# Optimization experiments

Measured on AMD Instinct MI355X. Metric: run time of the kernel, lower is better.

The kernel has to match this reference:

```python
import jax, jax.numpy as jnp
import numpy as np

E = 1024      # emb_dim
H = 16        # num_heads
DH = E // H   # per-head atten_dim
B = 2
T = 2048


def _layernorm(x, scale, shift, eps=1e-5):
    mean = x.mean(axis=-1, keepdims=True)
    var = ((x - mean) ** 2).mean(axis=-1, keepdims=True)  # unbiased=False
    return scale * (x - mean) / jnp.sqrt(var + eps) + shift


def _gelu(x):
    # Faithful to source: tanh(sqrt(2/pi)*x + 0.044715*x^3)  (no sqrt on cubic term)
    c = jnp.sqrt(jnp.asarray(2.0 / jnp.pi, x.dtype))
    return 0.5 * x * (1.0 + jnp.tanh(c * x + 0.044715 * x ** 3))


def setup_inputs() -> dict:
    key = jax.random.key(0)
    ks = jax.random.split(key, 12)
    s = 0.02
    return {
        "x":     jax.random.normal(ks[0], (B, T, E), jnp.float32),
        "Wq":    jax.random.normal(ks[1], (H, E, DH), jnp.float32) * s,
        "Wk":    jax.random.normal(ks[2], (H, E, DH), jnp.float32) * s,
        "Wv":    jax.random.normal(ks[3], (H, E, DH), jnp.float32) * s,
        "fc_w":  jax.random.normal(ks[4], (E, E), jnp.float32) * s,
        "fc_b":  jnp.zeros((E,), jnp.float32),
        "ln1_s": jnp.ones((E,), jnp.float32),
        "ln1_b": jnp.zeros((E,), jnp.float32),
        "ln2_s": jnp.ones((E,), jnp.float32),
        "ln2_b": jnp.zeros((E,), jnp.float32),
        "ff_w1": jax.random.normal(ks[5], (E, 4 * E), jnp.float32) * s,
        "ff_b1": jnp.zeros((4 * E,), jnp.float32),
        "ff_w2": jax.random.normal(ks[6], (4 * E, E), jnp.float32) * s,
        "ff_b2": jnp.zeros((E,), jnp.float32),
    }


def _attention(x, Wq, Wk, Wv, fc_w, fc_b):
    b, t, _ = x.shape
    q = jnp.einsum("bte,hed->bhtd", x, Wq)
    k = jnp.einsum("bte,hed->bhtd", x, Wk)
    v = jnp.einsum("bte,hed->bhtd", x, Wv)
    scores = jnp.einsum("bhtd,bhsd->bhts", q, k)
    causal = jnp.triu(jnp.ones((t, t), bool), 1)
    scores = jnp.where(causal, -jnp.inf, scores)
    w = jax.nn.softmax(scores / jnp.sqrt(jnp.asarray(DH, x.dtype)), axis=-1)
    ctx = jnp.einsum("bhts,bhsd->bhtd", w, v)
    # faithful quirk from source: per-head transpose(1,2) then reshape(b, T, d_out)
    ctx = jnp.swapaxes(ctx, 2, 3).reshape(b, H, t, DH)
    concat = ctx.transpose(0, 2, 1, 3).reshape(b, t, E)
    return concat @ fc_w + fc_b


def reference(x, Wq, Wk, Wv, fc_w, fc_b, ln1_s, ln1_b, ln2_s, ln2_b,
              ff_w1, ff_b1, ff_w2, ff_b2):
    h = _attention(_layernorm(x, ln1_s, ln1_b), Wq, Wk, Wv, fc_w, fc_b) + x
    y = _layernorm(h, ln2_s, ln2_b)
    y = _gelu(y @ ff_w1 + ff_b1) @ ff_w2 + ff_b2
    return y + h
```

## Files before the change

### kernel.cpp

```cpp
#include <hip/hip_runtime.h>


#define En 1024
#define Hn 16
#define DHn 64
#define Bn 2
#define Tn 2048
#define Mrows 4096

typedef __attribute__((ext_vector_type(8))) short bf16x8;
typedef __attribute__((ext_vector_type(4))) float f32x4;

__device__ __forceinline__ short f2bf(float f) {
    unsigned u = __float_as_uint(f);
    u += 0x7FFFu + ((u >> 16) & 1u);
    return (short)(u >> 16);
}
__device__ __forceinline__ ushort f2bfu(float f) {
    unsigned u = __float_as_uint(f);
    u += 0x7FFFu + ((u >> 16) & 1u);
    return (ushort)(u >> 16);
}

__device__ __forceinline__ float gelu_f(float x) {
    float u = 0.79788456080286535588f * x + 0.044715f * x * x * x;
    float t = __expf(2.0f * u);
    return x * t / (t + 1.0f);
}

__device__ __forceinline__ void load_lds16(const void* g, void* l) {
    __builtin_amdgcn_global_load_lds(
        (const __attribute__((address_space(1))) unsigned int*)(uintptr_t)g,
        (__attribute__((address_space(3))) unsigned int*)(uintptr_t)l,
        16, 0, 0);
}

__global__ __launch_bounds__(256) void ln_kernel(
    const float* __restrict__ in, const float* __restrict__ sc,
    const float* __restrict__ sh, ushort* __restrict__ out)
{
    int row = blockIdx.x;
    int tid = threadIdx.x;
    float4 v = ((const float4*)(in + (size_t)row * En))[tid];
    float s  = v.x + v.y + v.z + v.w;
    float s2 = v.x*v.x + v.y*v.y + v.z*v.z + v.w*v.w;
    #pragma unroll
    for (int off = 32; off > 0; off >>= 1) {
        s  += __shfl_down(s,  off);
        s2 += __shfl_down(s2, off);
    }
    __shared__ float red[2][4];
    int wave = tid >> 6, lane = tid & 63;
    if (lane == 0) { red[0][wave] = s; red[1][wave] = s2; }
    __syncthreads();
    s  = red[0][0] + red[0][1] + red[0][2] + red[0][3];
    s2 = red[1][0] + red[1][1] + red[1][2] + red[1][3];
    float mean = s * (1.0f / En);
    float var  = s2 * (1.0f / En) - mean * mean;
    float r = rsqrtf(var + 1e-5f);
    float4 scv = ((const float4*)sc)[tid];
    float4 shv = ((const float4*)sh)[tid];
    ushort4 o;
    o.x = f2bfu(scv.x * (v.x - mean) * r + shv.x);
    o.y = f2bfu(scv.y * (v.y - mean) * r + shv.y);
    o.z = f2bfu(scv.z * (v.z - mean) * r + shv.z);
    o.w = f2bfu(scv.w * (v.w - mean) * r + shv.w);
    ((ushort4*)(out + (size_t)row * En))[tid] = o;
}

__global__ __launch_bounds__(256) void ln2_fuse(
    const float* __restrict__ P0, const float* __restrict__ P1,
    const float* __restrict__ bias, const float* __restrict__ x,
    const float* __restrict__ sc, const float* __restrict__ sh,
    float* __restrict__ hb, ushort* __restrict__ ynb)
{
    int row = blockIdx.x, tid = threadIdx.x;
    size_t idx = (size_t)row * 256 + tid;
    float4 a  = ((const float4*)P0)[idx];
    float4 b  = ((const float4*)P1)[idx];
    float4 bi = ((const float4*)bias)[tid];
    float4 xr = ((const float4*)x)[idx];
    float4 v;
    v.x = a.x + b.x + bi.x + xr.x;
    v.y = a.y + b.y + bi.y + xr.y;
    v.z = a.z + b.z + bi.z + xr.z;
    v.w = a.w + b.w + bi.w + xr.w;
    ((float4*)hb)[idx] = v;
    float s  = v.x + v.y + v.z + v.w;
    float s2 = v.x*v.x + v.y*v.y + v.z*v.z + v.w*v.w;
    #pragma unroll
    for (int off = 32; off > 0; off >>= 1) {
        s  += __shfl_down(s,  off);
        s2 += __shfl_down(s2, off);
    }
    __shared__ float red[2][4];
    int wave = tid >> 6, lane = tid & 63;
    if (lane == 0) { red[0][wave] = s; red[1][wave] = s2; }
    __syncthreads();
    s  = red[0][0] + red[0][1] + red[0][2] + red[0][3];
    s2 = red[1][0] + red[1][1] + red[1][2] + red[1][3];
    float mean = s * (1.0f / En);
    float var  = s2 * (1.0f / En) - mean * mean;
    float r = rsqrtf(var + 1e-5f);
    float4 scv = ((const float4*)sc)[tid];
    float4 shv = ((const float4*)sh)[tid];
    ushort4 o;
    o.x = f2bfu(scv.x * (v.x - mean) * r + shv.x);
    o.y = f2bfu(scv.y * (v.y - mean) * r + shv.y);
    o.z = f2bfu(scv.z * (v.z - mean) * r + shv.z);
    o.w = f2bfu(scv.w * (v.w - mean) * r + shv.w);
    ((ushort4*)ynb)[idx] = o;
}

__global__ __launch_bounds__(256) void ff2_reduce(
    const float* __restrict__ P0, const float* __restrict__ P1,
    const float* __restrict__ bias, const float* __restrict__ hb,
    float* __restrict__ out)
{
    int tid = threadIdx.x;
    size_t i = (size_t)blockIdx.x * 256 + tid;
    float4 a  = ((const float4*)P0)[i];
    float4 b  = ((const float4*)P1)[i];
    float4 bi = ((const float4*)bias)[tid];
    float4 h  = ((const float4*)hb)[i];
    float4 o;
    o.x = a.x + b.x + bi.x + h.x;
    o.y = a.y + b.y + bi.y + h.y;
    o.z = a.z + b.z + bi.z + h.z;
    o.w = a.w + b.w + bi.w + h.w;
    ((float4*)out)[i] = o;
}

__global__ __launch_bounds__(256) void transpose_w(
    const float* __restrict__ in, ushort* __restrict__ out, int K, int N)
{
    __shared__ float t[64][65];
    int k0 = blockIdx.x * 64, n0 = blockIdx.y * 64;
    int tid = threadIdx.x, r = tid >> 4, c4 = (tid & 15) * 4;
    #pragma unroll
    for (int i = 0; i < 4; ++i) {
        float4 v = *(const float4*)(in + (size_t)(k0 + r + i * 16) * N + n0 + c4);
        t[r + i * 16][c4 + 0] = v.x; t[r + i * 16][c4 + 1] = v.y;
        t[r + i * 16][c4 + 2] = v.z; t[r + i * 16][c4 + 3] = v.w;
    }
    __syncthreads();
    #pragma unroll
    for (int i = 0; i < 4; ++i) {
        int n = r + i * 16;
        ushort4 u;
        u.x = f2bfu(t[c4 + 0][n]); u.y = f2bfu(t[c4 + 1][n]);
        u.z = f2bfu(t[c4 + 2][n]); u.w = f2bfu(t[c4 + 3][n]);
        *(ushort4*)(out + (size_t)(n0 + n) * K + k0 + c4) = u;
    }
}

__global__ __launch_bounds__(256) void transpose_qkv(
    const float* __restrict__ Wq, const float* __restrict__ Wk,
    const float* __restrict__ Wv, ushort* __restrict__ out)
{
    __shared__ float t[64][65];
    int z = blockIdx.z, sel = z >> 4, h = z & 15;
    const float* in = (sel == 0 ? Wq : sel == 1 ? Wk : Wv) + (size_t)h * En * DHn;
    ushort* o = out + ((size_t)(sel * 1024 + h * 64)) * En;
    int k0 = blockIdx.x * 64;
    int tid = threadIdx.x, r = tid >> 4, c4 = (tid & 15) * 4;
    #pragma unroll
    for (int i = 0; i < 4; ++i) {
        float4 v = *(const float4*)(in + (size_t)(k0 + r + i * 16) * DHn + c4);
        t[r + i * 16][c4 + 0] = v.x; t[r + i * 16][c4 + 1] = v.y;
        t[r + i * 16][c4 + 2] = v.z; t[r + i * 16][c4 + 3] = v.w;
    }
    __syncthreads();
    #pragma unroll
    for (int i = 0; i < 4; ++i) {
        int n = r + i * 16;
        ushort4 u;
        u.x = f2bfu(t[c4 + 0][n]); u.y = f2bfu(t[c4 + 1][n]);
        u.z = f2bfu(t[c4 + 2][n]); u.w = f2bfu(t[c4 + 3][n]);
        *(ushort4*)(o + (size_t)n * En + k0 + c4) = u;
    }
}

template<int MODE, int TN>
__global__ __launch_bounds__(256) void gemm_bf16(
    const ushort* __restrict__ A, int lda,
    const ushort* __restrict__ Bt, int ldb, int Kloop,
    const float* __restrict__ bias,
    float* __restrict__ Cf, ushort* __restrict__ Cb, int ldc,
    ushort* __restrict__ qo, ushort* __restrict__ ko, ushort* __restrict__ vo)
{
    constexpr int WCN = TN / 2;
    constexpr int NI  = WCN / 16;
    constexpr int BIW = TN * 8 / 256;
    __shared__ ushort As[128 * 64];
    __shared__ ushort Bs[TN * 64];
    int tid = threadIdx.x, wv = tid >> 6, lid = tid & 63;
    int m0 = blockIdx.x * 128, n0 = blockIdx.y * TN;
    int koff = blockIdx.z * Kloop;
    int wr = wv >> 1, wc = wv & 1;
    int hm = lid & 15, hk = lid >> 4;

    f32x4 acc[4][NI];
    #pragma unroll
    for (int i = 0; i < 4; ++i)
        #pragma unroll
        for (int j = 0; j < NI; ++j) acc[i][j] = (f32x4){0.f, 0.f, 0.f, 0.f};

    const ushort* Abase = A + (size_t)m0 * lda + koff;
    const ushort* Bbase = Bt + (size_t)n0 * ldb + koff;

    for (int k0 = 0; k0 < Kloop; k0 += 64) {
        __syncthreads();
        #pragma unroll
        for (int i = 0; i < 4; ++i) {
            int c = wv * 256 + i * 64 + lid;
            int r = c >> 3, s = c & 7;
            int j = s ^ (r & 7);
            load_lds16(Abase + (size_t)r * lda + k0 + j * 8,
                       &As[(wv * 256 + i * 64) * 8]);
        }
        #pragma unroll
        for (int i = 0; i < BIW; ++i) {
            int c = wv * (BIW * 64) + i * 64 + lid;
            int r = c >> 3, s = c & 7;
            int j = s ^ (r & 7);
            load_lds16(Bbase + (size_t)r * ldb + k0 + j * 8,
                       &Bs[(wv * (BIW * 64) + i * 64) * 8]);
        }
        __syncthreads();
        #pragma unroll
        for (int kk = 0; kk < 2; ++kk) {
            bf16x8 af[4], bfr[NI];
            #pragma unroll
            for (int mi = 0; mi < 4; ++mi) {
                int r = wr * 64 + mi * 16 + hm;
                int slot = ((kk << 2) | hk) ^ (r & 7);
                af[mi] = *(const bf16x8*)&As[(r * 8 + slot) * 8];
            }
            #pragma unroll
            for (int ni = 0; ni < NI; ++ni) {
                int r = wc * WCN + ni * 16 + hm;
                int slot = ((kk << 2) | hk) ^ (r & 7);
                bfr[ni] = *(const bf16x8*)&Bs[(r * 8 + slot) * 8];
            }
            #pragma unroll
            for (int mi = 0; mi < 4; ++mi)
                #pragma unroll
                for (int ni = 0; ni < NI; ++ni)
                    acc[mi][ni] = __builtin_amdgcn_mfma_f32_16x16x32_bf16(
                        af[mi], bfr[ni], acc[mi][ni], 0, 0, 0);
        }
    }

    int colbase = n0 + wc * WCN + hm;
    int rowbase = m0 + wr * 64 + hk * 4;
    if (MODE == 1) {
        #pragma unroll
        for (int ni = 0; ni < NI; ++ni) {
            int col = colbase + ni * 16;
            float bb = bias[col];
            #pragma unroll
            for (int mi = 0; mi < 4; ++mi) {
                int row = rowbase + mi * 16;
                #pragma unroll
                for (int r = 0; r < 4; ++r)
                    Cb[(size_t)(row + r) * ldc + col] =
                        f2bfu(gelu_f(acc[mi][ni][r] + bb));
            }
        }
    } else if (MODE == 2) {
        #pragma unroll
        for (int ni = 0; ni < NI; ++ni) {
            int col = colbase + ni * 16;
            int sel = col >> 10, cc = col & 1023;
            int h = cc >> 6, d = cc & 63;
            if (sel < 2) {
                ushort* outp = (sel == 0 ? qo : ko)
                             + (size_t)h * (Mrows * DHn) + d;
                #pragma unroll
                for (int mi = 0; mi < 4; ++mi) {
                    int row = rowbase + mi * 16;
                    #pragma unroll
                    for (int r = 0; r < 4; ++r)
                        outp[(size_t)(row + r) * DHn] = f2bfu(acc[mi][ni][r]);
                }
            } else {
                #pragma unroll
                for (int mi = 0; mi < 4; ++mi) {
                    int row = rowbase + mi * 16;
                    int bb2 = row >> 11, t = row & 2047;
                    ushort4 u;
                    u.x = f2bfu(acc[mi][ni][0]); u.y = f2bfu(acc[mi][ni][1]);
                    u.z = f2bfu(acc[mi][ni][2]); u.w = f2bfu(acc[mi][ni][3]);
                    *(ushort4*)(vo + ((size_t)((h * 2 + bb2) * 64 + d)) * Tn + t) = u;
                }
            }
        }
    } else {
        float* Cp = Cf + (size_t)blockIdx.z * Mrows * ldc;
        #pragma unroll
        for (int ni = 0; ni < NI; ++ni) {
            int col = colbase + ni * 16;
            #pragma unroll
            for (int mi = 0; mi < 4; ++mi) {
                int row = rowbase + mi * 16;
                #pragma unroll
                for (int r = 0; r < 4; ++r)
                    Cp[(size_t)(row + r) * ldc + col] = acc[mi][ni][r];
            }
        }
    }
}

__global__ __launch_bounds__(256) void attn_mfma(
    const ushort* __restrict__ q, const ushort* __restrict__ ksrc,
    const ushort* __restrict__ vtsrc, ushort* __restrict__ cat)
{
    int g = blockIdx.x;
    int h = g >> 1, b = g & 1;
    const ushort* qg  = q     + (size_t)g * Tn * DHn;
    const ushort* kg  = ksrc  + (size_t)g * Tn * DHn;
    const ushort* vtg = vtsrc + (size_t)g * DHn * Tn;
    int tid = threadIdx.x, wave = tid >> 6, lane = tid & 63;
    int m = lane & 15, gq = lane >> 4;

    __shared__ short Ks[4096];
    __shared__ short Vt[4096];
    __shared__ short Ps[4][1024];

    int R  = tid >> 2;
    int c2 = tid & 3;

    #pragma unroll 1
    for (int phase = 0; phase < 2; ++phase) {
        int qt = phase ? (31 - (int)blockIdx.y) : (int)blockIdx.y;
        int q0 = qt * 64;

        bf16x8 qf[2];
        {
            const ushort* qp = qg + (size_t)(q0 + wave * 16 + m) * DHn + gq * 8;
            qf[0] = *(const bf16x8*)(qp);
            qf[1] = *(const bf16x8*)(qp + 32);
        }
        f32x4 o[4];
        #pragma unroll
        for (int i = 0; i < 4; ++i) o[i] = (f32x4){0.f, 0.f, 0.f, 0.f};
        float lsum[4] = {0.f, 0.f, 0.f, 0.f};

        for (int kt = 0; kt <= qt; ++kt) {
            int k0 = kt * 64;
            __syncthreads();
            {
                const ushort* ksp = kg  + (size_t)(k0 + R) * DHn + c2 * 16;
                const ushort* vsp = vtg + (size_t)R * Tn + k0 + c2 * 16;
                bf16x8 f0 = *(const bf16x8*)(ksp);
                bf16x8 f1 = *(const bf16x8*)(ksp + 8);
                bf16x8 v0 = *(const bf16x8*)(vsp);
                bf16x8 v1 = *(const bf16x8*)(vsp + 8);
                *(bf16x8*)&Ks[R * 64 + (((c2 * 2    ) ^ (R & 7)) << 3)] = f0;
                *(bf16x8*)&Ks[R * 64 + (((c2 * 2 + 1) ^ (R & 7)) << 3)] = f1;
                *(bf16x8*)&Vt[R * 64 + (((c2 * 2    ) ^ (R & 7)) << 3)] = v0;
                *(bf16x8*)&Vt[R * 64 + (((c2 * 2 + 1) ^ (R & 7)) << 3)] = v1;
            }
            __syncthreads();

            bool diag = (kt == qt);
            float ps[4][4];
            #pragma unroll
            for (int ct = 0; ct < 4; ++ct) {
                if (diag && ct > wave) {
                    ps[ct][0] = ps[ct][1] = ps[ct][2] = ps[ct][3] = 0.f;
                    continue;
                }
                f32x4 acc = (f32x4){0.f, 0.f, 0.f, 0.f};
                int row = ct * 16 + m;
                #pragma unroll
                for (int db = 0; db < 2; ++db) {
                    bf16x8 kf = *(const bf16x8*)&Ks[row * 64 + (((db * 4 + gq) ^ (row & 7)) << 3)];
                    acc = __builtin_amdgcn_mfma_f32_16x16x32_bf16(qf[db], kf, acc, 0, 0, 0);
                }
                #pragma unroll
                for (int r = 0; r < 4; ++r) {
                    float p;
                    if (diag && (ct * 16 + m) > (wave * 16 + gq * 4 + r)) {
                        p = 0.f;
                    } else {
                        p = __expf(acc[r] * 0.125f);
                    }
                    ps[ct][r] = p;
                    lsum[r] += p;
                }
            }

            #pragma unroll
            for (int ct = 0; ct < 4; ++ct)
                #pragma unroll
                for (int r = 0; r < 4; ++r) {
                    int row = gq * 4 + r;
                    Ps[wave][row * 64 + ((((ct * 2 + (m >> 3)) ^ (row & 7)) << 3) | (m & 7))] =
                        f2bf(ps[ct][r]);
                }
            bf16x8 pf[2];
            #pragma unroll
            for (int db2 = 0; db2 < 2; ++db2)
                pf[db2] = *(const bf16x8*)&Ps[wave][m * 64 + (((db2 * 4 + gq) ^ (m & 7)) << 3)];

            #pragma unroll
            for (int ct2 = 0; ct2 < 4; ++ct2) {
                int row = ct2 * 16 + m;
                #pragma unroll
                for (int db2 = 0; db2 < 2; ++db2) {
                    bf16x8 vf = *(const bf16x8*)&Vt[row * 64 + (((db2 * 4 + gq) ^ (row & 7)) << 3)];
                    o[ct2] = __builtin_amdgcn_mfma_f32_16x16x32_bf16(pf[db2], vf, o[ct2], 0, 0, 0);
                }
            }
        }

        float inv[4];
        #pragma unroll
        for (int r = 0; r < 4; ++r) {
            float l = lsum[r];
            l += __shfl_xor(l, 1);
            l += __shfl_xor(l, 2);
            l += __shfl_xor(l, 4);
            l += __shfl_xor(l, 8);
            inv[r] = 1.0f / l;
        }
        size_t base = (size_t)b * Tn * En + (size_t)h * 64 + (size_t)qt * En
                    + wave * 16 + gq * 4;
        #pragma unroll
        for (int ct2 = 0; ct2 < 4; ++ct2) {
            int d = ct2 * 16 + m;
            #pragma unroll
            for (int r = 0; r < 4; ++r)
                cat[base + (size_t)d * 32 * En + r] = f2bfu(o[ct2][r] * inv[r]);
        }
    }
}

extern "C" void kernel_launch(void* const* d_in, const int* in_sizes, int n_in,
                              void* d_out, int out_size, void* d_ws, size_t ws_size,
                              hipStream_t stream) {
    const float* x     = (const float*)d_in[0];
    const float* Wq    = (const float*)d_in[1];
    const float* Wk    = (const float*)d_in[2];
    const float* Wv    = (const float*)d_in[3];
    const float* fc_w  = (const float*)d_in[4];
    const float* fc_b  = (const float*)d_in[5];
    const float* ln1_s = (const float*)d_in[6];
    const float* ln1_b = (const float*)d_in[7];
    const float* ln2_s = (const float*)d_in[8];
    const float* ln2_b = (const float*)d_in[9];
    const float* ff_w1 = (const float*)d_in[10];
    const float* ff_b1 = (const float*)d_in[11];
    const float* ff_w2 = (const float*)d_in[12];
    const float* ff_b2 = (const float*)d_in[13];
    float* out = (float*)d_out;
    (void)in_sizes; (void)n_in; (void)out_size; (void)ws_size;

    const size_t MB = 1048576;
    char* w8 = (char*)d_ws;
    ushort* S0   = (ushort*)(w8 + 0 * MB);
    ushort* kb   = (ushort*)(w8 + 8 * MB);
    ushort* vtb  = (ushort*)(w8 + 16 * MB);
    ushort* qb   = (ushort*)(w8 + 24 * MB);
    float*  hb   = (float*)(w8 + 32 * MB);
    ushort* y1   = (ushort*)(w8 + 48 * MB);
    float*  Pfc  = (float*)(w8 + 48 * MB);
    float*  Pff2 = (float*)(w8 + 0 * MB);
    ushort* wqkv = (ushort*)(w8 + 80 * MB);
    ushort* wfc  = (ushort*)(w8 + 86 * MB);
    ushort* wf1  = (ushort*)(w8 + 88 * MB);
    ushort* wf2  = (ushort*)(w8 + 96 * MB);

    transpose_qkv<<<dim3(16, 1, 48), 256, 0, stream>>>(Wq, Wk, Wv, wqkv);
    transpose_w<<<dim3(16, 16), 256, 0, stream>>>(fc_w, wfc, En, En);
    transpose_w<<<dim3(16, 64), 256, 0, stream>>>(ff_w1, wf1, En, 4 * En);
    transpose_w<<<dim3(64, 16), 256, 0, stream>>>(ff_w2, wf2, 4 * En, En);

    ln_kernel<<<dim3(Mrows), 256, 0, stream>>>(x, ln1_s, ln1_b, S0);
    gemm_bf16<2, 128><<<dim3(32, 24), 256, 0, stream>>>(
        S0, En, wqkv, En, En, nullptr, nullptr, nullptr, 0, qb, kb, vtb);
    attn_mfma<<<dim3(Hn * Bn, 16), 256, 0, stream>>>(qb, kb, vtb, S0);
    gemm_bf16<3, 64><<<dim3(32, 16, 2), 256, 0, stream>>>(
        S0, En, wfc, En, En / 2, nullptr, Pfc, nullptr, En, nullptr, nullptr, nullptr);
    ln2_fuse<<<dim3(Mrows), 256, 0, stream>>>(
        Pfc, Pfc + (size_t)Mrows * En, fc_b, x, ln2_s, ln2_b, hb, qb);
    gemm_bf16<1, 256><<<dim3(32, 16), 256, 0, stream>>>(
        qb, En, wf1, En, En, ff_b1, nullptr, y1, 4 * En, nullptr, nullptr, nullptr);
    gemm_bf16<3, 128><<<dim3(32, 8, 2), 256, 0, stream>>>(
        y1, 4 * En, wf2, 4 * En, 2 * En, nullptr, Pff2, nullptr, En, nullptr, nullptr, nullptr);
    ff2_reduce<<<dim3(Mrows), 256, 0, stream>>>(
        Pff2, Pff2 + (size_t)Mrows * En, ff_b2, hb, out);
}
```

Baseline: 375.4 us.

## Stage QKV epilogue through LDS, store residual as bf16, shrink FF tiles

The QKV GEMM epilogue now writes each wave's tile into padded shared memory and then issues coalesced 8-byte stores for Q/K and the transposed V. Before, it used scattered 2-byte stores. The residual h buffer is stored in bf16 instead of fp32, which halves its write and read traffic in ln2_fuse and ff2_reduce but adds rounding error to the final residual add. The FF1 and FF2 GEMMs switch to smaller N tiles with more blocks, trading per-block reuse for more parallelism.

After: 353.5 us. 1.06x faster.

```diff
diff --git a/kernel.cpp b/kernel.cpp
--- a/kernel.cpp
+++ b/kernel.cpp
@@ -20,6 +20,9 @@
     unsigned u = __float_as_uint(f);
     u += 0x7FFFu + ((u >> 16) & 1u);
     return (ushort)(u >> 16);
+}
+__device__ __forceinline__ float bf2f(ushort u) {
+    return __uint_as_float((unsigned)u << 16);
 }
 
 __device__ __forceinline__ float gelu_f(float x) {
@@ -72,7 +75,7 @@
     const float* __restrict__ P0, const float* __restrict__ P1,
     const float* __restrict__ bias, const float* __restrict__ x,
     const float* __restrict__ sc, const float* __restrict__ sh,
-    float* __restrict__ hb, ushort* __restrict__ ynb)
+    ushort* __restrict__ hb, ushort* __restrict__ ynb)
 {
     int row = blockIdx.x, tid = threadIdx.x;
     size_t idx = (size_t)row * 256 + tid;
@@ -85,7 +88,9 @@
     v.y = a.y + b.y + bi.y + xr.y;
     v.z = a.z + b.z + bi.z + xr.z;
     v.w = a.w + b.w + bi.w + xr.w;
-    ((float4*)hb)[idx] = v;
+    ushort4 hv;
+    hv.x = f2bfu(v.x); hv.y = f2bfu(v.y); hv.z = f2bfu(v.z); hv.w = f2bfu(v.w);
+    ((ushort4*)hb)[idx] = hv;
     float s  = v.x + v.y + v.z + v.w;
     float s2 = v.x*v.x + v.y*v.y + v.z*v.z + v.w*v.w;
     #pragma unroll
@@ -114,7 +119,7 @@
 
 __global__ __launch_bounds__(256) void ff2_reduce(
     const float* __restrict__ P0, const float* __restrict__ P1,
-    const float* __restrict__ bias, const float* __restrict__ hb,
+    const float* __restrict__ bias, const ushort* __restrict__ hb,
     float* __restrict__ out)
 {
     int tid = threadIdx.x;
@@ -122,12 +127,12 @@
     float4 a  = ((const float4*)P0)[i];
     float4 b  = ((const float4*)P1)[i];
     float4 bi = ((const float4*)bias)[tid];
-    float4 h  = ((const float4*)hb)[i];
+    ushort4 hu = ((const ushort4*)hb)[i];
     float4 o;
-    o.x = a.x + b.x + bi.x + h.x;
-    o.y = a.y + b.y + bi.y + h.y;
-    o.z = a.z + b.z + bi.z + h.z;
-    o.w = a.w + b.w + bi.w + h.w;
+    o.x = a.x + b.x + bi.x + bf2f(hu.x);
+    o.y = a.y + b.y + bi.y + bf2f(hu.y);
+    o.z = a.z + b.z + bi.z + bf2f(hu.z);
+    o.w = a.w + b.w + bi.w + bf2f(hu.w);
     ((float4*)out)[i] = o;
 }
 
@@ -192,8 +197,11 @@
     constexpr int WCN = TN / 2;
     constexpr int NI  = WCN / 16;
     constexpr int BIW = TN * 8 / 256;
-    __shared__ ushort As[128 * 64];
-    __shared__ ushort Bs[TN * 64];
+    constexpr int STAGE = 128 * 64 + TN * 64;
+    constexpr int SMEMN = (MODE == 2 && STAGE < 4 * 64 * 68) ? 4 * 64 * 68 : STAGE;
+    __shared__ ushort smem[SMEMN];
+    ushort* As = smem;
+    ushort* Bs = smem + 128 * 64;
     int tid = threadIdx.x, wv = tid >> 6, lid = tid & 63;
     int m0 = blockIdx.x * 128, n0 = blockIdx.y * TN;
     int koff = blockIdx.z * Kloop;
@@ -269,31 +277,45 @@
             }
         }
     } else if (MODE == 2) {
-        #pragma unroll
-        for (int ni = 0; ni < NI; ++ni) {
-            int col = colbase + ni * 16;
-            int sel = col >> 10, cc = col & 1023;
-            int h = cc >> 6, d = cc & 63;
-            if (sel < 2) {
-                ushort* outp = (sel == 0 ? qo : ko)
-                             + (size_t)h * (Mrows * DHn) + d;
-                #pragma unroll
-                for (int mi = 0; mi < 4; ++mi) {
-                    int row = rowbase + mi * 16;
+        __syncthreads();
+        ushort* Ls = smem + wv * (64 * 68);
+        int col0 = n0 + wc * 64;
+        int sel = col0 >> 10, h = (col0 & 1023) >> 6;
+        if (sel < 2) {
+            #pragma unroll
+            for (int ni = 0; ni < NI; ++ni)
+                #pragma unroll
+                for (int mi = 0; mi < 4; ++mi)
                     #pragma unroll
                     for (int r = 0; r < 4; ++r)
-                        outp[(size_t)(row + r) * DHn] = f2bfu(acc[mi][ni][r]);
-                }
-            } else {
-                #pragma unroll
-                for (int mi = 0; mi < 4; ++mi) {
-                    int row = rowbase + mi * 16;
-                    int bb2 = row >> 11, t = row & 2047;
-                    ushort4 u;
-                    u.x = f2bfu(acc[mi][ni][0]); u.y = f2bfu(acc[mi][ni][1]);
-                    u.z = f2bfu(acc[mi][ni][2]); u.w = f2bfu(acc[mi][ni][3]);
-                    *(ushort4*)(vo + ((size_t)((h * 2 + bb2) * 64 + d)) * Tn + t) = u;
-                }
+                        Ls[(mi * 16 + hk * 4 + r) * 68 + ni * 16 + hm] =
+                            f2bfu(acc[mi][ni][r]);
+            ushort* outp = (sel == 0 ? qo : ko) + (size_t)h * (Mrows * DHn);
+            int dcol = hm * 4;
+            #pragma unroll
+            for (int i = 0; i < 16; ++i) {
+                int t = hk + i * 4;
+                *(ushort4*)(outp + (size_t)(m0 + wr * 64 + t) * DHn + dcol) =
+                    *(const ushort4*)&Ls[t * 68 + dcol];
+            }
+        } else {
+            #pragma unroll
+            for (int ni = 0; ni < NI; ++ni)
+                #pragma unroll
+                for (int mi = 0; mi < 4; ++mi)
+                    #pragma unroll
+                    for (int r = 0; r < 4; ++r)
+                        Ls[(ni * 16 + hm) * 68 + mi * 16 + hk * 4 + r] =
+                            f2bfu(acc[mi][ni][r]);
+            int bb2 = m0 >> 11;
+            int t0 = (m0 & 2047) + wr * 64;
+            ushort* outp = vo + ((size_t)((h * 2 + bb2) * 64)) * Tn + t0;
+            int tcol = hm * 4;
+            #pragma unroll
+            for (int i = 0; i < 16; ++i) {
+                int d = hk + i * 4;
+                *(ushort4*)(outp + (size_t)d * Tn + tcol) =
+                    *(const ushort4*)&Ls[d * 68 + tcol];
             }
         }
     } else {
@@ -464,7 +486,7 @@
     ushort* kb   = (ushort*)(w8 + 8 * MB);
     ushort* vtb  = (ushort*)(w8 + 16 * MB);
     ushort* qb   = (ushort*)(w8 + 24 * MB);
-    float*  hb   = (float*)(w8 + 32 * MB);
+    ushort* hb   = (ushort*)(w8 + 32 * MB);
     ushort* y1   = (ushort*)(w8 + 48 * MB);
     float*  Pfc  = (float*)(w8 + 48 * MB);
     float*  Pff2 = (float*)(w8 + 0 * MB);
@@ -486,9 +508,9 @@
         S0, En, wfc, En, En / 2, nullptr, Pfc, nullptr, En, nullptr, nullptr, nullptr);
     ln2_fuse<<<dim3(Mrows), 256, 0, stream>>>(
         Pfc, Pfc + (size_t)Mrows * En, fc_b, x, ln2_s, ln2_b, hb, qb);
-    gemm_bf16<1, 256><<<dim3(32, 16), 256, 0, stream>>>(
+    gemm_bf16<1, 128><<<dim3(32, 32), 256, 0, stream>>>(
         qb, En, wf1, En, En, ff_b1, nullptr, y1, 4 * En, nullptr, nullptr, nullptr);
-    gemm_bf16<3, 128><<<dim3(32, 8, 2), 256, 0, stream>>>(
+    gemm_bf16<3, 64><<<dim3(32, 16, 2), 256, 0, stream>>>(
         y1, 4 * En, wf2, 4 * En, 2 * En, nullptr, Pff2, nullptr, En, nullptr, nullptr, nullptr);
     ff2_reduce<<<dim3(Mrows), 256, 0, stream>>>(
         Pff2, Pff2 + (size_t)Mrows * En, ff_b2, hb, out);
```
